# Optimization experiments

Hardware: AMD Instinct MI355X
Metric: run time of the kernel (lower is better)

## Reference

```python
import jax, jax.numpy as jnp
import numpy as np

N_HEAD = 12
D_HEAD = 64
ROT_DIM = 32
THETA = 10000.0
LOOK_B = 1
LOOK_F = 1


def _rope(t):
    # t: [b, h, n, d]; interleaved RoPE on first ROT_DIM dims (lucidrains convention)
    n = t.shape[-2]
    inv_freq = 1.0 / (THETA ** (jnp.arange(0, ROT_DIM, 2, dtype=jnp.float32) / ROT_DIM))
    freqs = jnp.arange(n, dtype=jnp.float32)[:, None] * inv_freq[None, :]   # [n, ROT_DIM//2]
    freqs = jnp.repeat(freqs, 2, axis=-1)                                   # [n, ROT_DIM]
    cos, sin = jnp.cos(freqs), jnp.sin(freqs)
    t_rot, t_pass = t[..., :ROT_DIM], t[..., ROT_DIM:]
    pair = t_rot.reshape(*t_rot.shape[:-1], ROT_DIM // 2, 2)
    rot = jnp.stack([-pair[..., 1], pair[..., 0]], axis=-1).reshape(t_rot.shape)
    return jnp.concatenate([t_rot * cos + rot * sin, t_pass], axis=-1)


def _look_around(x, backward=LOOK_B, forward=LOOK_F, pad_value=-1, dim=2):
    # x: [B, w, n, ...]; pad the window axis, gather shifted windows, concat along dim
    w = x.shape[1]
    pad_width = [(0, 0)] * x.ndim
    pad_width[1] = (backward, forward)
    padded = jnp.pad(x, pad_width, constant_values=pad_value)
    return jnp.concatenate([padded[:, i:i + w] for i in range(forward + backward + 1)], axis=dim)


def _forward(x, w_attn, b_attn, window_size):
    b, n, d_model = x.shape
    qkv = x @ w_attn + b_attn                       # [b, n, 3*d_model]
    q, k, v = jnp.split(qkv, 3, axis=-1)

    def split_heads(t):
        return t.reshape(b, n, N_HEAD, D_HEAD).transpose(0, 2, 1, 3)  # [b, h, n, dh]

    q, k, v = split_heads(q), split_heads(k), split_heads(v)
    q, k = _rope(q), _rope(k)

    scale = D_HEAD ** -0.5
    B = b * N_HEAD
    w = n // window_size
    bq = q.reshape(B, w, window_size, D_HEAD) * scale
    bk = _look_around(k.reshape(B, w, window_size, D_HEAD), pad_value=-1.0)
    bv = _look_around(v.reshape(B, w, window_size, D_HEAD), pad_value=-1.0)

    seq = jnp.arange(n).reshape(1, w, window_size)
    bq_k = _look_around(seq, pad_value=-1)          # [1, w, (lb+lf+1)*ws]
    pad_mask = (bq_k == -1)[:, :, None, :]          # [1, w, 1, j]

    sim = jnp.einsum('bwie,bwje->bwij', bq, bk)     # [B, w, ws, (lb+lf+1)*ws]
    sim = jnp.where(pad_mask, -jnp.finfo(sim.dtype).max, sim)
    attn = jax.nn.softmax(sim, axis=-1)
    out = jnp.einsum('bwij,bwje->bwie', attn, bv)   # [B, w, ws, dh]
    out = out.reshape(b, N_HEAD, n, D_HEAD).transpose(0, 2, 1, 3).reshape(b, n, N_HEAD * D_HEAD)
    return out


def setup_inputs() -> dict:
    key = jax.random.key(0)
    k1, k2, k3 = jax.random.split(key, 3)
    d_model = 768
    x = jax.random.normal(k1, (4, 4096, d_model), dtype=jnp.float32)
    w_attn = jax.random.normal(k2, (d_model, 3 * d_model), dtype=jnp.float32) * 0.02
    b_attn = jax.random.normal(k3, (3 * d_model,), dtype=jnp.float32) * 0.02
    return {"x": x, "w_attn": w_attn, "b_attn": b_attn, "window_size": 128}


def reference(x, w_attn, b_attn, window_size):
    return _forward(x, w_attn, b_attn, window_size)
```

## Files before the change

kernel.cpp:

```cpp
#include <hip/hip_runtime.h>

typedef __attribute__((ext_vector_type(8))) short short8;
typedef __attribute__((ext_vector_type(16))) float f32x16;
typedef __attribute__((ext_vector_type(4))) float f32x4;

#define L2T 13.287712379549449f

__device__ __forceinline__ unsigned short f2bf(float f) {
  unsigned int u = __float_as_uint(f);
  u += 0x7FFFu + ((u >> 16) & 1u);
  return (unsigned short)(u >> 16);
}
__device__ __forceinline__ float bf2f(unsigned short u) {
  return __uint_as_float(((unsigned int)u) << 16);
}

__device__ __forceinline__ void gload16(const unsigned short* g, unsigned short* l) {
  __builtin_amdgcn_global_load_lds(
      (const __attribute__((address_space(1))) void*)g,
      (__attribute__((address_space(3))) void*)l, 16, 0, 0);
}

__global__ __launch_bounds__(256) void prep_kernel(const float* __restrict__ x,
                                                   unsigned short* __restrict__ xb,
                                                   const float* __restrict__ w,
                                                   unsigned short* __restrict__ wt) {
  __shared__ float tile[32][33];
  int bid = blockIdx.x;
  if (bid < 12288) {
    int i = bid * 256 + threadIdx.x;
    float4 v = ((const float4*)x)[i];
    ushort4 o;
    o.x = f2bf(v.x); o.y = f2bf(v.y); o.z = f2bf(v.z); o.w = f2bf(v.w);
    ((ushort4*)xb)[i] = o;
  } else {
    int b2 = bid - 12288;
    int n0 = (b2 % 72) * 32, k0 = (b2 / 72) * 32;
    int tx = threadIdx.x & 31, ty = threadIdx.x >> 5;
    for (int i = ty; i < 32; i += 8)
      tile[i][tx] = w[(size_t)(k0 + i) * 2304 + n0 + tx];
    __syncthreads();
    for (int i = ty; i < 32; i += 8)
      wt[(size_t)(n0 + i) * 768 + k0 + tx] = f2bf(tile[tx][i]);
  }
}

__global__ __launch_bounds__(256) void qkv_gemm_kernel(
    const unsigned short* __restrict__ xb,
    const unsigned short* __restrict__ wt,
    const float* __restrict__ bias,
    unsigned short* __restrict__ Qb,
    unsigned short* __restrict__ Kb,
    unsigned short* __restrict__ Vb) {
  __shared__ unsigned short lA[128 * 64];
  __shared__ unsigned short lB[128 * 64];
  int bid = blockIdx.x;
  int swz = (bid & 7) * 288 + (bid >> 3);
  int mt = swz / 18, nt = swz - mt * 18;
  int m0 = mt * 128, n0 = nt * 128;

  int tid = threadIdx.x;
  int lane = tid & 63, wid = tid >> 6;
  int wr = wid >> 1, wc = wid & 1;
  int lr = lane & 15, lg = lane >> 4;
  int lswz = lr & 7;

  int offA[4], offB[4];
  unsigned short* ldsA[4];
  unsigned short* ldsB[4];
#pragma unroll
  for (int i = 0; i < 4; i++) {
    int gi = (wid * 4 + i) * 64 + lane;
    int r = gi >> 3;
    int gcl = (gi & 7) ^ (r & 7);
    offA[i] = (m0 + r) * 768 + gcl * 8;
    offB[i] = (n0 + r) * 768 + gcl * 8;
    ldsA[i] = &lA[(wid * 4 + i) * 512];
    ldsB[i] = &lB[(wid * 4 + i) * 512];
  }

  f32x4 acc[4][4] = {};
  const int rowA = (wr * 64 + lr) * 64;
  const int rowB = (wc * 64 + lr) * 64;

  for (int k0 = 0; k0 < 768; k0 += 64) {
    __syncthreads();
#pragma unroll
    for (int i = 0; i < 4; i++) gload16(xb + offA[i] + k0, ldsA[i]);
#pragma unroll
    for (int i = 0; i < 4; i++) gload16(wt + offB[i] + k0, ldsB[i]);
    __syncthreads();

    short8 af[4][2], bfr[4][2];
#pragma unroll
    for (int ks = 0; ks < 2; ks++) {
      int c = ((ks * 4 + lg) ^ lswz) * 8;
#pragma unroll
      for (int mi = 0; mi < 4; mi++)
        af[mi][ks] = *(const short8*)(&lA[rowA + mi * 1024 + c]);
#pragma unroll
      for (int ni = 0; ni < 4; ni++)
        bfr[ni][ks] = *(const short8*)(&lB[rowB + ni * 1024 + c]);
    }
#pragma unroll
    for (int ks = 0; ks < 2; ks++)
#pragma unroll
      for (int mi = 0; mi < 4; mi++)
#pragma unroll
        for (int ni = 0; ni < 4; ni++)
          acc[mi][ni] = __builtin_amdgcn_mfma_f32_16x16x32_bf16(af[mi][ks], bfr[ni][ks], acc[mi][ni], 0, 0, 0);
  }

#pragma unroll
  for (int ni = 0; ni < 4; ni++) {
    int n = n0 + wc * 64 + ni * 16 + lr;
    float bv = bias[n];
    int which = n / 768;
    int idx = n - which * 768;
    int h = idx >> 6, d = idx & 63;
    unsigned short* dst = (which == 0) ? Qb : ((which == 1) ? Kb : Vb);
#pragma unroll
    for (int mi = 0; mi < 4; mi++) {
#pragma unroll
      for (int reg = 0; reg < 4; reg++) {
        int m = m0 + wr * 64 + mi * 16 + lg * 4 + reg;
        int b = m >> 12, t = m & 4095;
        dst[(((size_t)(b * 12 + h)) * 4096 + t) * 64 + d] = f2bf(acc[mi][ni][reg] + bv);
      }
    }
  }
}

#define KV_S 72
__global__ __launch_bounds__(256) void attn_kernel(
    const unsigned short* __restrict__ Qb,
    const unsigned short* __restrict__ Kb,
    const unsigned short* __restrict__ Vb,
    float* __restrict__ out) {
  __shared__ unsigned short kS[64 * KV_S];
  __shared__ unsigned short vS[64 * KV_S];
  int wi = blockIdx.x;
  int bh = blockIdx.y;
  int b = bh / 12, h = bh - b * 12;
  int tid = threadIdx.x, lane = tid & 63, wid = tid >> 6;
  int l31 = lane & 31, hi = lane >> 5;

  int qb0 = wi * 128 + wid * 32;
  const unsigned short* Qrow = Qb + ((size_t)bh * 4096 + qb0) * 64;
  short8 qf[4];
#pragma unroll
  for (int kk = 0; kk < 4; kk++)
    qf[kk] = *(const short8*)(Qrow + (size_t)l31 * 64 + kk * 16 + hi * 8);

  {
    int t = qb0 + l31;
#pragma unroll
    for (int kk = 0; kk < 2; kk++) {
      unsigned short* e = (unsigned short*)&qf[kk];
      int j0 = kk * 8 + hi * 4;
#pragma unroll
      for (int p = 0; p < 4; p++) {
        float invf = exp2f(-(float)(j0 + p) * (L2T / 16.0f));
        float ang = (float)t * invf;
        float s, c;
        __sincosf(ang, &s, &c);
        float a = bf2f(e[2 * p]), b2 = bf2f(e[2 * p + 1]);
        e[2 * p] = f2bf(a * c - b2 * s);
        e[2 * p + 1] = f2bf(b2 * c + a * s);
      }
    }
  }

  f32x16 oacc[2];
#pragma unroll
  for (int dt = 0; dt < 2; dt++)
#pragma unroll
    for (int r = 0; r < 16; r++) oacc[dt][r] = 0.0f;
  float mrow = -1e30f, lsum = 0.0f;

  const unsigned short* Kbase = Kb + (size_t)bh * 4096 * 64;
  const unsigned short* Vbase = Vb + (size_t)bh * 4096 * 64;

  int vk = tid & 63;
  int vq = tid >> 6;

  for (int c = 0; c < 6; c++) {
    int kp0 = (wi - 1) * 128 + c * 64;
    if (kp0 < 0 || kp0 >= 4096) continue;

    __syncthreads();
#pragma unroll
    for (int ci = tid; ci < 512; ci += 256) {
      int kk = ci >> 3, co = (ci & 7) * 8;
      uint4 val = *(const uint4*)(Kbase + (size_t)(kp0 + kk) * 64 + co);
      if (co < 32) {
        unsigned short* e = (unsigned short*)&val;
        int t = kp0 + kk;
        int j0 = co >> 1;
#pragma unroll
        for (int p = 0; p < 4; p++) {
          float invf = exp2f(-(float)(j0 + p) * (L2T / 16.0f));
          float ang = (float)t * invf;
          float s, cc;
          __sincosf(ang, &s, &cc);
          float a = bf2f(e[2 * p]), b2 = bf2f(e[2 * p + 1]);
          e[2 * p] = f2bf(a * cc - b2 * s);
          e[2 * p + 1] = f2bf(b2 * cc + a * s);
        }
      }
      *(uint4*)(&kS[kk * KV_S + co]) = val;
    }
    {
      const unsigned short* vp = Vbase + (size_t)(kp0 + vk) * 64 + vq * 16;
      uint4 v0 = *(const uint4*)(vp);
      uint4 v1 = *(const uint4*)(vp + 8);
      const unsigned short* e = (const unsigned short*)&v0;
#pragma unroll
      for (int i = 0; i < 8; i++) vS[(vq * 16 + i) * KV_S + vk] = e[i];
      e = (const unsigned short*)&v1;
#pragma unroll
      for (int i = 0; i < 8; i++) vS[(vq * 16 + 8 + i) * KV_S + vk] = e[i];
    }
    __syncthreads();

    f32x16 s[2];
#pragma unroll
    for (int kt = 0; kt < 2; kt++) {
      f32x16 acc;
#pragma unroll
      for (int r = 0; r < 16; r++) acc[r] = 0.0f;
#pragma unroll
      for (int kk = 0; kk < 4; kk++) {
        short8 kf = *(const short8*)(&kS[(kt * 32 + l31) * KV_S + kk * 16 + hi * 8]);
        acc = __builtin_amdgcn_mfma_f32_32x32x16_bf16(kf, qf[kk], acc, 0, 0, 0);
      }
      s[kt] = acc;
    }
#pragma unroll
    for (int kt = 0; kt < 2; kt++)
#pragma unroll
      for (int r = 0; r < 16; r++) s[kt][r] *= 0.125f;

    float vmax = -1e30f;
#pragma unroll
    for (int kt = 0; kt < 2; kt++)
#pragma unroll
      for (int r = 0; r < 16; r++) vmax = fmaxf(vmax, s[kt][r]);
    vmax = fmaxf(vmax, __shfl_xor(vmax, 32, 64));
    float mnew = fmaxf(mrow, vmax);
    float corr = __expf(mrow - mnew);
    mrow = mnew;
    float rs = 0.0f;
#pragma unroll
    for (int kt = 0; kt < 2; kt++)
#pragma unroll
      for (int r = 0; r < 16; r++) {
        float p = __expf(s[kt][r] - mnew);
        s[kt][r] = p;
        rs += p;
      }
    rs += __shfl_xor(rs, 32, 64);
    lsum = lsum * corr + rs;
#pragma unroll
    for (int dt = 0; dt < 2; dt++)
#pragma unroll
      for (int r = 0; r < 16; r++) oacc[dt][r] *= corr;

#pragma unroll
    for (int kt = 0; kt < 2; kt++) {
#pragma unroll
      for (int kk = 0; kk < 2; kk++) {
        unsigned a0, a1, b0, b1;
        asm("v_cvt_pk_bf16_f32 %0, %1, %2" : "=v"(a0) : "v"(s[kt][kk * 8 + 0]), "v"(s[kt][kk * 8 + 1]));
        asm("v_cvt_pk_bf16_f32 %0, %1, %2" : "=v"(a1) : "v"(s[kt][kk * 8 + 2]), "v"(s[kt][kk * 8 + 3]));
        asm("v_cvt_pk_bf16_f32 %0, %1, %2" : "=v"(b0) : "v"(s[kt][kk * 8 + 4]), "v"(s[kt][kk * 8 + 5]));
        asm("v_cvt_pk_bf16_f32 %0, %1, %2" : "=v"(b1) : "v"(s[kt][kk * 8 + 6]), "v"(s[kt][kk * 8 + 7]));
        asm("v_permlane32_swap_b32 %0, %1" : "+v"(a0), "+v"(b0));
        asm("v_permlane32_swap_b32 %0, %1" : "+v"(a1), "+v"(b1));
        union { unsigned u[4]; short8 v; } pb;
        pb.u[0] = a0; pb.u[1] = a1; pb.u[2] = b0; pb.u[3] = b1;
#pragma unroll
        for (int dt = 0; dt < 2; dt++) {
          short8 vf = *(const short8*)(&vS[(dt * 32 + l31) * KV_S + kt * 32 + kk * 16 + hi * 8]);
          oacc[dt] = __builtin_amdgcn_mfma_f32_32x32x16_bf16(vf, pb.v, oacc[dt], 0, 0, 0);
        }
      }
    }
  }

  float inv = 1.0f / lsum;
  float* orow = out + ((size_t)b * 4096 + qb0 + l31) * 768 + h * 64;
#pragma unroll
  for (int dt = 0; dt < 2; dt++)
#pragma unroll
    for (int g = 0; g < 4; g++) {
      float4 o;
      o.x = oacc[dt][g * 4 + 0] * inv;
      o.y = oacc[dt][g * 4 + 1] * inv;
      o.z = oacc[dt][g * 4 + 2] * inv;
      o.w = oacc[dt][g * 4 + 3] * inv;
      *(float4*)(orow + dt * 32 + g * 8 + hi * 4) = o;
    }
}

extern "C" void kernel_launch(void* const* d_in, const int* in_sizes, int n_in,
                              void* d_out, int out_size, void* d_ws, size_t ws_size,
                              hipStream_t stream) {
  const float* x = (const float*)d_in[0];
  const float* w = (const float*)d_in[1];
  const float* bias = (const float*)d_in[2];
  float* out = (float*)d_out;

  char* ws = (char*)d_ws;
  unsigned short* xb = (unsigned short*)ws;
  unsigned short* wt = (unsigned short*)(ws + 25165824);
  unsigned short* Qb = (unsigned short*)(ws + 28704768);
  unsigned short* Kb = Qb + 12582912;
  unsigned short* Vb = Kb + 12582912;

  hipLaunchKernelGGL(prep_kernel, dim3(14016), dim3(256), 0, stream, x, xb, w, wt);
  hipLaunchKernelGGL(qkv_gemm_kernel, dim3(2304), dim3(256), 0, stream, xb, wt, bias, Qb, Kb, Vb);
  hipLaunchKernelGGL(attn_kernel, dim3(32, 48), dim3(256), 0, stream, Qb, Kb, Vb, out);
}
```

Before: 152.2 us.

## Precompute K RoPE in a separate pass and swizzle attention block order

Moves the rotary embedding of K out of the attention kernel into a dedicated pass that rotates every K row once in place. Previously each key chunk was rotated up to three times, once by each neighbouring window's block that loaded it. The change also remaps blockIdx.x to the window index so blocks sharing K/V windows are scheduled in a different order, which may affect L2 reuse. The cost is an extra kernel launch plus a full read and write of K in memory.

```diff
diff --git a/kernel.cpp b/kernel.cpp
--- a/kernel.cpp
+++ b/kernel.cpp
@@ -131,6 +131,28 @@
   }
 }
 
+__global__ __launch_bounds__(256) void krope_kernel(unsigned short* __restrict__ Kb) {
+  int r = blockIdx.x * 256 + threadIdx.x;
+  int t = r & 4095;
+  unsigned short* p = Kb + (size_t)r * 64;
+  uint4 raw[4];
+#pragma unroll
+  for (int i = 0; i < 4; i++) raw[i] = ((uint4*)p)[i];
+  unsigned short* us = (unsigned short*)raw;
+#pragma unroll
+  for (int j = 0; j < 16; j++) {
+    float invf = exp2f(-(float)j * (L2T / 16.0f));
+    float ang = (float)t * invf;
+    float s, c;
+    __sincosf(ang, &s, &c);
+    float a = bf2f(us[2 * j]), b = bf2f(us[2 * j + 1]);
+    us[2 * j] = f2bf(a * c - b * s);
+    us[2 * j + 1] = f2bf(b * c + a * s);
+  }
+#pragma unroll
+  for (int i = 0; i < 4; i++) ((uint4*)p)[i] = raw[i];
+}
+
 #define KV_S 72
 __global__ __launch_bounds__(256) void attn_kernel(
     const unsigned short* __restrict__ Qb,
@@ -139,7 +161,8 @@
     float* __restrict__ out) {
   __shared__ unsigned short kS[64 * KV_S];
   __shared__ unsigned short vS[64 * KV_S];
-  int wi = blockIdx.x;
+  int bidx = blockIdx.x;
+  int wi = ((bidx & 7) << 2) | (bidx >> 3);
   int bh = blockIdx.y;
   int b = bh / 12, h = bh - b * 12;
   int tid = threadIdx.x, lane = tid & 63, wid = tid >> 6;
@@ -192,23 +215,7 @@
 #pragma unroll
     for (int ci = tid; ci < 512; ci += 256) {
       int kk = ci >> 3, co = (ci & 7) * 8;
-      uint4 val = *(const uint4*)(Kbase + (size_t)(kp0 + kk) * 64 + co);
-      if (co < 32) {
-        unsigned short* e = (unsigned short*)&val;
-        int t = kp0 + kk;
-        int j0 = co >> 1;
-#pragma unroll
-        for (int p = 0; p < 4; p++) {
-          float invf = exp2f(-(float)(j0 + p) * (L2T / 16.0f));
-          float ang = (float)t * invf;
-          float s, cc;
-          __sincosf(ang, &s, &cc);
-          float a = bf2f(e[2 * p]), b2 = bf2f(e[2 * p + 1]);
-          e[2 * p] = f2bf(a * cc - b2 * s);
-          e[2 * p + 1] = f2bf(b2 * cc + a * s);
-        }
-      }
-      *(uint4*)(&kS[kk * KV_S + co]) = val;
+      *(uint4*)(&kS[kk * KV_S + co]) = *(const uint4*)(Kbase + (size_t)(kp0 + kk) * 64 + co);
     }
     {
       const unsigned short* vp = Vbase + (size_t)(kp0 + vk) * 64 + vq * 16;
@@ -320,5 +327,6 @@
 
   hipLaunchKernelGGL(prep_kernel, dim3(14016), dim3(256), 0, stream, x, xb, w, wt);
   hipLaunchKernelGGL(qkv_gemm_kernel, dim3(2304), dim3(256), 0, stream, xb, wt, bias, Qb, Kb, Vb);
+  hipLaunchKernelGGL(krope_kernel, dim3(768), dim3(256), 0, stream, Kb);
   hipLaunchKernelGGL(attn_kernel, dim3(32, 48), dim3(256), 0, stream, Qb, Kb, Vb, out);
 }
```

New measurement: 143.9 us. 5.4% less time.
